# Kernel tuning notes

Hardware: AMD Instinct MI355X
Metric: run time of the kernel (lower is better)

Reference implementation:

```python
import jax, jax.numpy as jnp
import numpy as np
from jax import lax

NUM_FILTERS = 180
DN = ('NCHW', 'OIHW', 'NCHW')


def _gabor_kernel(freq, theta, sigma_x, sigma_y, n_stds=3):
    # real part of skimage.filters.gabor_kernel
    ct, st = np.cos(theta), np.sin(theta)
    x0 = int(np.ceil(max(abs(n_stds * sigma_x * ct), abs(n_stds * sigma_y * st), 1)))
    y0 = int(np.ceil(max(abs(n_stds * sigma_y * ct), abs(n_stds * sigma_x * st), 1)))
    y, x = np.mgrid[-y0:y0 + 1, -x0:x0 + 1]
    rotx = x * ct + y * st
    roty = -x * st + y * ct
    g = np.exp(-0.5 * (rotx ** 2 / sigma_x ** 2 + roty ** 2 / sigma_y ** 2))
    g /= 2.0 * np.pi * sigma_x * sigma_y
    return g * np.cos(2.0 * np.pi * freq * rotx)  # Re{exp(1j*2*pi*f*rotx)}


def _make_weights(sigma_x, sigma_y, freq, num_filters):
    kernels = [
        _gabor_kernel(freq, theta=np.pi - th, sigma_x=sigma_x, sigma_y=sigma_y)
        for th in np.linspace(0, np.pi * (num_filters - 1) / num_filters, num_filters)
    ]
    s = max(max(k.shape) for k in kernels)  # 17 for defaults
    kernels = np.stack([
        np.pad(k, [[(s - k.shape[0]) // 2], [(s - k.shape[1]) // 2]]) for k in kernels
    ])
    return kernels.astype(np.float32)


def _gauss1d(sigma, truncate=4.0):
    # matches scipy.ndimage gaussian kernel (skimage default truncate=4.0)
    r = int(truncate * sigma + 0.5)
    xs = np.arange(-r, r + 1, dtype=np.float64)
    k = np.exp(-0.5 * (xs / sigma) ** 2)
    return (k / k.sum()).astype(np.float32), r


def _gaussian_blur(img, sigma):
    # separable blur with edge-replicate ('nearest') padding, img: [B,1,H,W]
    k, r = _gauss1d(sigma)
    kh = jnp.asarray(k).reshape(1, 1, -1, 1)
    kw = jnp.asarray(k).reshape(1, 1, 1, -1)
    p = jnp.pad(img, ((0, 0), (0, 0), (r, r), (0, 0)), mode='edge')
    img = lax.conv_general_dilated(p, kh, (1, 1), 'VALID', dimension_numbers=DN)
    p = jnp.pad(img, ((0, 0), (0, 0), (0, 0), (r, r)), mode='edge')
    return lax.conv_general_dilated(p, kw, (1, 1), 'VALID', dimension_numbers=DN)


def setup_inputs() -> dict:
    key = jax.random.key(0)
    x = jax.random.uniform(key, (2, 3, 512, 512), dtype=jnp.float32)
    weights = jnp.asarray(_make_weights(1.8, 2.4, 0.23, NUM_FILTERS))[:, None, :, :]  # [180,1,17,17]
    bins = jnp.asarray(
        np.linspace(0, np.pi * (NUM_FILTERS - 1) / NUM_FILTERS, NUM_FILTERS), jnp.float32
    ).reshape(1, -1, 1, 1)
    return {'x': x, 'weights': weights, 'bins': bins}


def reference(x, weights, bins):
    # rgb -> gray, [B,1,H,W]
    gray = (0.2989 * x[:, 0] + 0.587 * x[:, 1] + 0.114 * x[:, 2])[:, None]
    # difference of gaussians (skimage, low=0.4, high=10.0)
    filtered = _gaussian_blur(gray, 0.4) - _gaussian_blur(gray, 10.0)
    kh, kw = weights.shape[2], weights.shape[3]
    response = lax.conv_general_dilated(
        filtered, weights, (1, 1), ((kh // 2, kh // 2), (kw // 2, kw // 2)),
        dimension_numbers=DN)  # [B,180,H,W]
    response = jnp.abs(response)
    idx = jnp.argmax(response, axis=1)[:, None]  # [B,1,H,W]
    orientation_map = idx.astype(jnp.float32) / NUM_FILTERS * 255.0
    orientation_map_rad = orientation_map / NUM_FILTERS * jnp.pi
    d0 = jnp.abs(orientation_map_rad - bins)
    dists = jnp.minimum(d0, jnp.minimum(jnp.abs(orientation_map_rad - bins - jnp.pi),
                                        jnp.abs(orientation_map_rad - bins + jnp.pi)))
    F_orients_norm = response / jnp.sum(response, axis=1, keepdims=True)
    confidence_map = jnp.sum(dists ** 2 * F_orients_norm, axis=1)  # [B,H,W]
    return orientation_map, confidence_map
```

## Files before the change

### kernel.cpp

```cpp
#include <hip/hip_runtime.h>
#include <math.h>
#include <stdint.h>

#define H 512
#define W 512
#define NPIX (H * W)
#define NB 2
#define NF 180
#define KS 17
#define WSCALE 1024.0f

#define RAW_OFF 0
#define BB_OFF  1600
#define BCH_U32 3072
#define PH_U32  (2 * BCH_U32)
#define POOL_U32 (1600 + 2 * PH_U32)

typedef _Float16 half8 __attribute__((ext_vector_type(8)));
typedef float floatx16 __attribute__((ext_vector_type(16)));
typedef uint32_t u32x4 __attribute__((ext_vector_type(4)));

union FragU { u32x4 u; half8 h; };

__device__ inline void gl_lds16(const uint32_t* g, uint32_t* l) {
  __builtin_amdgcn_global_load_lds((const __attribute__((address_space(1))) void*)g,
                                   (__attribute__((address_space(3))) void*)l, 16, 0, 0);
}

__global__ void k_taps(float* __restrict__ taps) {
  if (threadIdx.x == 0 && blockIdx.x == 0) {
    {
      double k[5], s = 0.0;
      for (int i = 0; i < 5; i++) { double xv = (double)(i - 2) / 0.4; k[i] = exp(-0.5 * xv * xv); s += k[i]; }
      for (int i = 0; i < 5; i++) taps[i] = (float)(k[i] / s);
    }
    {
      double k[81], s = 0.0;
      for (int i = 0; i < 81; i++) { double xv = (double)(i - 40) / 10.0; k[i] = exp(-0.5 * xv * xv); s += k[i]; }
      for (int i = 0; i < 81; i++) taps[8 + i] = (float)(k[i] / s);
    }
  }
}

__global__ void k_repackB(const float* __restrict__ w, uint32_t* __restrict__ Bf) {
  int tid = blockIdx.x * 256 + threadIdx.x;
  if (tid >= 19 * 6 * 64 * 4) return;
  int q = tid & 3;
  int lane = (tid >> 2) & 63;
  int ct = tid >> 8;
  int t = ct % 6, c = ct / 6;
  int n = t * 32 + (lane & 31);
  int hf = lane >> 5;
  uint32_t hv = 0, lv = 0;
  for (int s = 0; s < 2; s++) {
    int j = 2 * q + s;
    int k = hf * 8 + j;
    float val = 0.f;
    if (n < NF) {
      if (c < 17)       val = w[n * 289 + c * 17 + k];
      else if (c == 17) val = w[n * 289 + k * 17 + 16];
      else if (k == 0)  val = w[n * 289 + 16 * 17 + 16];
    }
    val *= WSCALE;
    _Float16 hh = (_Float16)val;
    _Float16 ll = (_Float16)(val - (float)hh);
    hv |= (uint32_t)__builtin_bit_cast(uint16_t, hh) << (16 * s);
    lv |= (uint32_t)__builtin_bit_cast(uint16_t, ll) << (16 * s);
  }
  int base = c * 3072;
  int off = t * 256 + lane * 4 + q;
  Bf[base + off] = hv;
  Bf[base + 1536 + off] = lv;
}

__global__ void k_gray(const float* __restrict__ x, float* __restrict__ gray) {
  int i = blockIdx.x * blockDim.x + threadIdx.x;
  if (i >= NB * NPIX) return;
  int b = i / NPIX, r = i % NPIX;
  const float* xb = x + (size_t)b * 3 * NPIX;
  gray[i] = 0.2989f * xb[r] + 0.587f * xb[NPIX + r] + 0.114f * xb[2 * NPIX + r];
}

__global__ void k_vblur2(const float* __restrict__ in, float* __restrict__ outA,
                         float* __restrict__ outB, const float* __restrict__ taps) {
  int i = blockIdx.x * blockDim.x + threadIdx.x;
  if (i >= NB * NPIX) return;
  int b = i / NPIX, r = i % NPIX;
  int y = r / W, xx = r % W;
  const float* img = in + (size_t)b * NPIX;
  float a = 0.f;
#pragma unroll
  for (int j = -2; j <= 2; j++) {
    int yy = y + j; yy = yy < 0 ? 0 : (yy > H - 1 ? H - 1 : yy);
    a = fmaf(taps[j + 2], img[yy * W + xx], a);
  }
  float c = 0.f;
  for (int j = -40; j <= 40; j++) {
    int yy = y + j; yy = yy < 0 ? 0 : (yy > H - 1 ? H - 1 : yy);
    c = fmaf(taps[8 + j + 40], img[yy * W + xx], c);
  }
  outA[i] = a;
  outB[i] = c;
}

__global__ void k_hblur_dog(const float* __restrict__ inA, const float* __restrict__ inB,
                            uint32_t* __restrict__ dogp, const float* __restrict__ taps) {
  int i = blockIdx.x * blockDim.x + threadIdx.x;
  if (i >= NB * NPIX) return;
  int b = i / NPIX, r = i % NPIX;
  int y = r / W, xx = r % W;
  const float* ra = inA + (size_t)b * NPIX + (size_t)y * W;
  const float* rb = inB + (size_t)b * NPIX + (size_t)y * W;
  float a = 0.f;
#pragma unroll
  for (int j = -2; j <= 2; j++) {
    int xc = xx + j; xc = xc < 0 ? 0 : (xc > W - 1 ? W - 1 : xc);
    a = fmaf(taps[j + 2], ra[xc], a);
  }
  float c = 0.f;
  for (int j = -40; j <= 40; j++) {
    int xc = xx + j; xc = xc < 0 ? 0 : (xc > W - 1 ? W - 1 : xc);
    c = fmaf(taps[8 + j + 40], rb[xc], c);
  }
  float d = a - c;
  _Float16 hh = (_Float16)d;
  _Float16 ll = (_Float16)(d - (float)hh);
  dogp[i] = ((uint32_t)__builtin_bit_cast(uint16_t, ll) << 16) |
            (uint32_t)__builtin_bit_cast(uint16_t, hh);
}

__launch_bounds__(256, 1)
__global__ void k_conv(const uint32_t* __restrict__ dogp,
                       const uint32_t* __restrict__ Bf,
                       const float* __restrict__ bins,
                       float* __restrict__ out) {
  __shared__ uint32_t pool[POOL_U32];

  const int b  = blockIdx.z;
  const int y0 = blockIdx.y * 4;
  const int x0 = blockIdx.x * 64;
  const int tid = threadIdx.x;
  const int lane = tid & 63;
  const int w  = __builtin_amdgcn_readfirstlane(tid >> 6);
  const int rp2 = (w >> 1) * 2;
  const int ch  = w & 1;
  const int nl = lane & 31;
  const int half = lane >> 5;

  const uint32_t* dgb = dogp + (size_t)b * NPIX;
  for (int i = tid; i < 20 * 80; i += 256) {
    int ry = i / 80, rx = i % 80;
    int gy = y0 + ry - 8, gx = x0 + rx - 8;
    uint32_t v = 0;
    if (gy >= 0 && gy < H && gx >= 0 && gx < W) v = dgb[gy * W + gx];
    pool[RAW_OFF + i] = v;
  }
  {
    const uint32_t* src = Bf + (size_t)tid * 4;
    uint32_t* dst = &pool[BB_OFF + tid * 4];
#pragma unroll
    for (int i = 0; i < 6; i++) gl_lds16(src + i * 1024, dst + i * 1024);
  }
  asm volatile("s_waitcnt vmcnt(0)" ::: "memory");
  __syncthreads();

  floatx16 acc[2][6];
#pragma unroll
  for (int d = 0; d < 2; d++)
#pragma unroll
    for (int t = 0; t < 6; t++)
#pragma unroll
      for (int q = 0; q < 16; q++) acc[d][t][q] = 0.f;

  const int abase = ch * 32 + nl + half * 8;

  auto buildRow = [&](int tr, FragU& fh, FragU& fl) {
    const uint32_t* rp = &pool[RAW_OFF + tr * 80 + abase];
    uint32_t d[8];
#pragma unroll
    for (int j = 0; j < 8; j++) d[j] = rp[j];
#pragma unroll
    for (int q = 0; q < 4; q++) {
      fh.u[q] = __builtin_amdgcn_perm(d[2 * q + 1], d[2 * q], 0x05040100u);
      fl.u[q] = __builtin_amdgcn_perm(d[2 * q + 1], d[2 * q], 0x07060302u);
    }
  };
  auto buildStrip = [&](int c, int rb, FragU& fh, FragU& fl) {
    int kyb = (c - 17) * 16 + half * 8;
    uint32_t d[8];
#pragma unroll
    for (int j = 0; j < 8; j++) {
      int ky = kyb + j; if (ky > 16) ky = 16;
      d[j] = pool[RAW_OFF + (rb + ky) * 80 + ch * 32 + nl + 16];
    }
#pragma unroll
    for (int q = 0; q < 4; q++) {
      fh.u[q] = __builtin_amdgcn_perm(d[2 * q + 1], d[2 * q], 0x05040100u);
      fl.u[q] = __builtin_amdgcn_perm(d[2 * q + 1], d[2 * q], 0x07060302u);
    }
  };
  auto halfChunk = [&](int off, int t0, FragU& d0h, FragU& d0l, FragU& d1h, FragU& d1l) {
    FragU wh[3], wl[3];
#pragma unroll
    for (int t = 0; t < 3; t++) {
      wh[t].u = *(const u32x4*)&pool[off + (t0 + t) * 256 + lane * 4];
      wl[t].u = *(const u32x4*)&pool[off + 1536 + (t0 + t) * 256 + lane * 4];
    }
#pragma unroll
    for (int t = 0; t < 3; t++) {
      acc[0][t0 + t] = __builtin_amdgcn_mfma_f32_32x32x16_f16(wh[t].h, d0h.h, acc[0][t0 + t], 0, 0, 0);
      acc[1][t0 + t] = __builtin_amdgcn_mfma_f32_32x32x16_f16(wh[t].h, d1h.h, acc[1][t0 + t], 0, 0, 0);
    }
#pragma unroll
    for (int t = 0; t < 3; t++) {
      acc[0][t0 + t] = __builtin_amdgcn_mfma_f32_32x32x16_f16(wh[t].h, d0l.h, acc[0][t0 + t], 0, 0, 0);
      acc[1][t0 + t] = __builtin_amdgcn_mfma_f32_32x32x16_f16(wh[t].h, d1l.h, acc[1][t0 + t], 0, 0, 0);
    }
#pragma unroll
    for (int t = 0; t < 3; t++) {
      acc[0][t0 + t] = __builtin_amdgcn_mfma_f32_32x32x16_f16(wl[t].h, d0h.h, acc[0][t0 + t], 0, 0, 0);
      acc[1][t0 + t] = __builtin_amdgcn_mfma_f32_32x32x16_f16(wl[t].h, d1h.h, acc[1][t0 + t], 0, 0, 0);
    }
  };
  auto mfmaChunk = [&](int off, FragU& d0h, FragU& d0l, FragU& d1h, FragU& d1l) {
    halfChunk(off, 0, d0h, d0l, d1h, d1l);
    halfChunk(off, 3, d0h, d0l, d1h, d1l);
  };

  FragU a0h, a0l, a1h, a1l;
  buildRow(rp2, a0h, a0l);

  int buf = 0;
  for (int p = 0; p < 8; p++) {
    {
      const uint32_t* src = Bf + (size_t)(2 * p + 2) * BCH_U32 + (size_t)tid * 4;
      uint32_t* dst = &pool[BB_OFF + (buf ^ 1) * PH_U32 + tid * 4];
#pragma unroll
      for (int i = 0; i < 6; i++) gl_lds16(src + i * 1024, dst + i * 1024);
    }
    buildRow(rp2 + 1 + 2 * p, a1h, a1l);
    mfmaChunk(BB_OFF + buf * PH_U32, a0h, a0l, a1h, a1l);
    a0h = a1h; a0l = a1l;
    buildRow(rp2 + 2 + 2 * p, a1h, a1l);
    mfmaChunk(BB_OFF + buf * PH_U32 + BCH_U32, a0h, a0l, a1h, a1l);
    a0h = a1h; a0l = a1l;

    asm volatile("s_waitcnt vmcnt(0)" ::: "memory");
    __syncthreads();
    buf ^= 1;
  }

  {
    const uint32_t* src = Bf + (size_t)18 * BCH_U32 + (size_t)tid * 4;
    uint32_t* dst = &pool[BB_OFF + (buf ^ 1) * PH_U32 + tid * 4];
#pragma unroll
    for (int i = 0; i < 3; i++) gl_lds16(src + i * 1024, dst + i * 1024);

    buildRow(rp2 + 17, a1h, a1l);
    mfmaChunk(BB_OFF + buf * PH_U32, a0h, a0l, a1h, a1l);

    FragU s0h, s0l, s1h, s1l;
    buildStrip(17, rp2, s0h, s0l);
    buildStrip(17, rp2 + 1, s1h, s1l);
    mfmaChunk(BB_OFF + buf * PH_U32 + BCH_U32, s0h, s0l, s1h, s1l);

    asm volatile("s_waitcnt vmcnt(0)" ::: "memory");
    __syncthreads();
    buf ^= 1;
  }
  {
    FragU s0h, s0l, s1h, s1l;
    buildStrip(18, rp2, s0h, s0l);
    buildStrip(18, rp2 + 1, s1h, s1l);
    mfmaChunk(BB_OFF + buf * PH_U32, s0h, s0l, s1h, s1l);
  }

  const float PI_F = 3.14159265358979323846f;
  const float INV_PI = 0.31830988618379067154f;
  const double STEPD = 3.14159265358979323846 * 179.0 / 180.0 / 179.0;
  const float stepf = (float)STEPD;
  const float hbase = (4.0f * (float)half) * stepf;

#pragma unroll
  for (int d = 0; d < 2; d++) {
    float m = -1.f; int n = 0; float S0 = 0.f, S1 = 0.f;
#pragma unroll
    for (int t = 0; t < 6; t++) {
#pragma unroll
      for (int q = 0; q < 16; q++) {
        float v = fabsf(acc[d][t][q]);
        if (q & 1) S1 += v; else S0 += v;
        int nf = 32 * t + (q & 3) + 8 * (q >> 2) + 4 * half;
        if (v > m) { m = v; n = nf; }
      }
    }
    float S = S0 + S1;
    {
      float mo = __shfl_xor(m, 32);
      int   no = __shfl_xor(n, 32);
      float So = __shfl_xor(S, 32);
      bool take = (mo > m) || (mo == m && no < n);
      if (take) { m = mo; n = no; }
      S += So;
    }
    float om  = (float)n / 180.0f * 255.0f;
    float rad = om / 180.0f * PI_F;
    float ddc = rad - hbase;
    float C0 = 0.f, C1 = 0.f;
#pragma unroll
    for (int t = 0; t < 6; t++) {
#pragma unroll
      for (int q = 0; q < 16; q++) {
        const float K = (float)((double)(32 * t + (q & 3) + 8 * (q >> 2)) * STEPD);
        float dd = ddc - K;
        float r = rintf(dd * INV_PI);
        float dist = fmaf(-PI_F, r, dd);
        float w2 = dist * dist;
        if (q & 1) C1 = fmaf(w2, fabsf(acc[d][t][q]), C1);
        else       C0 = fmaf(w2, fabsf(acc[d][t][q]), C0);
      }
    }
    float C = C0 + C1;
    C += __shfl_xor(C, 32);
    if (half == 0) {
      int y = y0 + rp2 + d;
      int x = x0 + ch * 32 + nl;
      out[(size_t)b * NPIX + (size_t)y * W + x] = om;
      out[(size_t)NB * NPIX + (size_t)b * NPIX + (size_t)y * W + x] = C / S;
    }
  }
}

extern "C" void kernel_launch(void* const* d_in, const int* in_sizes, int n_in,
                              void* d_out, int out_size, void* d_ws, size_t ws_size,
                              hipStream_t stream) {
  const float* x = (const float*)d_in[0];
  const float* wts = (const float*)d_in[1];
  const float* bins = (const float*)d_in[2];
  float* out = (float*)d_out;

  float* ws = (float*)d_ws;
  float* gray = ws;
  float* tmpA = ws + (size_t)NB * NPIX;
  float* tmpB = tmpA + (size_t)NB * NPIX;
  uint32_t* dogp = (uint32_t*)(tmpB + (size_t)NB * NPIX);
  float* taps = (float*)(dogp + (size_t)NB * NPIX);
  uint32_t* Bf = (uint32_t*)(taps + 128);

  k_taps<<<1, 64, 0, stream>>>(taps);
  k_repackB<<<114, 256, 0, stream>>>(wts, Bf);

  int n = NB * NPIX;
  int blk = 256, grd = (n + blk - 1) / blk;
  k_gray<<<grd, blk, 0, stream>>>(x, gray);
  k_vblur2<<<grd, blk, 0, stream>>>(gray, tmpA, tmpB, taps);
  k_hblur_dog<<<grd, blk, 0, stream>>>(tmpA, tmpB, dogp, taps);

  dim3 g(W / 64, H / 4, NB);
  k_conv<<<g, 256, 0, stream>>>(dogp, Bf, bins, out);
}
```

Baseline: 200.4 us.

## Split filter bank across two wave groups with LDS cross-wave reduction

The conv kernel now runs 512 threads per block, and each wave handles half of the 180 filters (3 of the 6 MFMA tiles) instead of all of them. This halves the accumulator registers per wave and doubles the wave count, which should raise occupancy and latency hiding. The price is an LDS-based argmax/sum merge between filter groups and extra block barriers. The weight staging loads are redistributed across the larger thread count.

Measured after the change: 193.8 us. 3.3% less time.

```diff
diff --git a/kernel.cpp b/kernel.cpp
--- a/kernel.cpp
+++ b/kernel.cpp
@@ -129,7 +129,7 @@
             (uint32_t)__builtin_bit_cast(uint16_t, hh);
 }
 
-__launch_bounds__(256, 1)
+__launch_bounds__(512, 2)
 __global__ void k_conv(const uint32_t* __restrict__ dogp,
                        const uint32_t* __restrict__ Bf,
                        const float* __restrict__ bins,
@@ -142,13 +142,14 @@
   const int tid = threadIdx.x;
   const int lane = tid & 63;
   const int w  = __builtin_amdgcn_readfirstlane(tid >> 6);
-  const int rp2 = (w >> 1) * 2;
-  const int ch  = w & 1;
+  const int fg  = w & 1;
+  const int ch  = (w >> 1) & 1;
+  const int rp2 = (w >> 2) * 2;
   const int nl = lane & 31;
   const int half = lane >> 5;
 
   const uint32_t* dgb = dogp + (size_t)b * NPIX;
-  for (int i = tid; i < 20 * 80; i += 256) {
+  for (int i = tid; i < 20 * 80; i += 512) {
     int ry = i / 80, rx = i % 80;
     int gy = y0 + ry - 8, gx = x0 + rx - 8;
     uint32_t v = 0;
@@ -159,16 +160,16 @@
     const uint32_t* src = Bf + (size_t)tid * 4;
     uint32_t* dst = &pool[BB_OFF + tid * 4];
 #pragma unroll
-    for (int i = 0; i < 6; i++) gl_lds16(src + i * 1024, dst + i * 1024);
+    for (int i = 0; i < 3; i++) gl_lds16(src + i * 2048, dst + i * 2048);
   }
   asm volatile("s_waitcnt vmcnt(0)" ::: "memory");
   __syncthreads();
 
-  floatx16 acc[2][6];
+  floatx16 acc[2][3];
 #pragma unroll
   for (int d = 0; d < 2; d++)
 #pragma unroll
-    for (int t = 0; t < 6; t++)
+    for (int t = 0; t < 3; t++)
 #pragma unroll
       for (int q = 0; q < 16; q++) acc[d][t][q] = 0.f;
 
@@ -199,32 +200,28 @@
       fl.u[q] = __builtin_amdgcn_perm(d[2 * q + 1], d[2 * q], 0x07060302u);
     }
   };
-  auto halfChunk = [&](int off, int t0, FragU& d0h, FragU& d0l, FragU& d1h, FragU& d1l) {
+  auto mfmaChunk = [&](int off, FragU& d0h, FragU& d0l, FragU& d1h, FragU& d1l) {
     FragU wh[3], wl[3];
 #pragma unroll
     for (int t = 0; t < 3; t++) {
-      wh[t].u = *(const u32x4*)&pool[off + (t0 + t) * 256 + lane * 4];
-      wl[t].u = *(const u32x4*)&pool[off + 1536 + (t0 + t) * 256 + lane * 4];
-    }
-#pragma unroll
-    for (int t = 0; t < 3; t++) {
-      acc[0][t0 + t] = __builtin_amdgcn_mfma_f32_32x32x16_f16(wh[t].h, d0h.h, acc[0][t0 + t], 0, 0, 0);
-      acc[1][t0 + t] = __builtin_amdgcn_mfma_f32_32x32x16_f16(wh[t].h, d1h.h, acc[1][t0 + t], 0, 0, 0);
-    }
-#pragma unroll
-    for (int t = 0; t < 3; t++) {
-      acc[0][t0 + t] = __builtin_amdgcn_mfma_f32_32x32x16_f16(wh[t].h, d0l.h, acc[0][t0 + t], 0, 0, 0);
-      acc[1][t0 + t] = __builtin_amdgcn_mfma_f32_32x32x16_f16(wh[t].h, d1l.h, acc[1][t0 + t], 0, 0, 0);
-    }
-#pragma unroll
-    for (int t = 0; t < 3; t++) {
-      acc[0][t0 + t] = __builtin_amdgcn_mfma_f32_32x32x16_f16(wl[t].h, d0h.h, acc[0][t0 + t], 0, 0, 0);
-      acc[1][t0 + t] = __builtin_amdgcn_mfma_f32_32x32x16_f16(wl[t].h, d1h.h, acc[1][t0 + t], 0, 0, 0);
-    }
-  };
-  auto mfmaChunk = [&](int off, FragU& d0h, FragU& d0l, FragU& d1h, FragU& d1l) {
-    halfChunk(off, 0, d0h, d0l, d1h, d1l);
-    halfChunk(off, 3, d0h, d0l, d1h, d1l);
+      wh[t].u = *(const u32x4*)&pool[off + (3 * fg + t) * 256 + lane * 4];
+      wl[t].u = *(const u32x4*)&pool[off + 1536 + (3 * fg + t) * 256 + lane * 4];
+    }
+#pragma unroll
+    for (int t = 0; t < 3; t++) {
+      acc[0][t] = __builtin_amdgcn_mfma_f32_32x32x16_f16(wh[t].h, d0h.h, acc[0][t], 0, 0, 0);
+      acc[1][t] = __builtin_amdgcn_mfma_f32_32x32x16_f16(wh[t].h, d1h.h, acc[1][t], 0, 0, 0);
+    }
+#pragma unroll
+    for (int t = 0; t < 3; t++) {
+      acc[0][t] = __builtin_amdgcn_mfma_f32_32x32x16_f16(wh[t].h, d0l.h, acc[0][t], 0, 0, 0);
+      acc[1][t] = __builtin_amdgcn_mfma_f32_32x32x16_f16(wh[t].h, d1l.h, acc[1][t], 0, 0, 0);
+    }
+#pragma unroll
+    for (int t = 0; t < 3; t++) {
+      acc[0][t] = __builtin_amdgcn_mfma_f32_32x32x16_f16(wl[t].h, d0h.h, acc[0][t], 0, 0, 0);
+      acc[1][t] = __builtin_amdgcn_mfma_f32_32x32x16_f16(wl[t].h, d1h.h, acc[1][t], 0, 0, 0);
+    }
   };
 
   FragU a0h, a0l, a1h, a1l;
@@ -236,7 +233,7 @@
       const uint32_t* src = Bf + (size_t)(2 * p + 2) * BCH_U32 + (size_t)tid * 4;
       uint32_t* dst = &pool[BB_OFF + (buf ^ 1) * PH_U32 + tid * 4];
 #pragma unroll
-      for (int i = 0; i < 6; i++) gl_lds16(src + i * 1024, dst + i * 1024);
+      for (int i = 0; i < 3; i++) gl_lds16(src + i * 2048, dst + i * 2048);
     }
     buildRow(rp2 + 1 + 2 * p, a1h, a1l);
     mfmaChunk(BB_OFF + buf * PH_U32, a0h, a0l, a1h, a1l);
@@ -253,8 +250,8 @@
   {
     const uint32_t* src = Bf + (size_t)18 * BCH_U32 + (size_t)tid * 4;
     uint32_t* dst = &pool[BB_OFF + (buf ^ 1) * PH_U32 + tid * 4];
-#pragma unroll
-    for (int i = 0; i < 3; i++) gl_lds16(src + i * 1024, dst + i * 1024);
+    gl_lds16(src, dst);
+    if (tid < 256) gl_lds16(src + 2048, dst + 2048);
 
     buildRow(rp2 + 17, a1h, a1l);
     mfmaChunk(BB_OFF + buf * PH_U32, a0h, a0l, a1h, a1l);
@@ -274,44 +271,80 @@
     buildStrip(18, rp2 + 1, s1h, s1l);
     mfmaChunk(BB_OFF + buf * PH_U32, s0h, s0l, s1h, s1l);
   }
+  __syncthreads();
+
+  float* pm = (float*)&pool[0];
+  int*   pn = (int*)&pool[512];
+  float* pS = (float*)&pool[1024];
+  float* pc = (float*)&pool[1536];
+  int*   fn = (int*)&pool[2048];
+  float* fS = (float*)&pool[2304];
 
   const float PI_F = 3.14159265358979323846f;
   const float INV_PI = 0.31830988618379067154f;
   const double STEPD = 3.14159265358979323846 * 179.0 / 180.0 / 179.0;
   const float stepf = (float)STEPD;
   const float hbase = (4.0f * (float)half) * stepf;
+  const int colp = ch * 32 + nl;
 
 #pragma unroll
   for (int d = 0; d < 2; d++) {
     float m = -1.f; int n = 0; float S0 = 0.f, S1 = 0.f;
 #pragma unroll
-    for (int t = 0; t < 6; t++) {
+    for (int t = 0; t < 3; t++) {
 #pragma unroll
       for (int q = 0; q < 16; q++) {
         float v = fabsf(acc[d][t][q]);
         if (q & 1) S1 += v; else S0 += v;
-        int nf = 32 * t + (q & 3) + 8 * (q >> 2) + 4 * half;
+        int nf = 32 * (3 * fg + t) + (q & 3) + 8 * (q >> 2) + 4 * half;
         if (v > m) { m = v; n = nf; }
       }
     }
     float S = S0 + S1;
-    {
-      float mo = __shfl_xor(m, 32);
-      int   no = __shfl_xor(n, 32);
-      float So = __shfl_xor(S, 32);
-      bool take = (mo > m) || (mo == m && no < n);
-      if (take) { m = mo; n = no; }
-      S += So;
-    }
-    float om  = (float)n / 180.0f * 255.0f;
+    float mo = __shfl_xor(m, 32);
+    int   no = __shfl_xor(n, 32);
+    float So = __shfl_xor(S, 32);
+    bool take = (mo > m) || (mo == m && no < n);
+    if (take) { m = mo; n = no; }
+    S += So;
+    if (half == 0) {
+      int o = ((rp2 + d) * 2 + fg) * 64 + colp;
+      pm[o] = m; pn[o] = n; pS[o] = S;
+    }
+  }
+  __syncthreads();
+
+  if (fg == 0) {
+#pragma unroll
+    for (int d = 0; d < 2; d++) {
+      int rd = rp2 + d;
+      int o0 = (rd * 2 + 0) * 64 + colp;
+      int o1 = (rd * 2 + 1) * 64 + colp;
+      float m0 = pm[o0], m1 = pm[o1];
+      int n = (m1 > m0) ? pn[o1] : pn[o0];
+      float S = pS[o0] + pS[o1];
+      float om = (float)n / 180.0f * 255.0f;
+      if (half == 0) {
+        fn[rd * 64 + colp] = n; fS[rd * 64 + colp] = S;
+        out[(size_t)b * NPIX + (size_t)(y0 + rd) * W + x0 + colp] = om;
+      }
+    }
+  }
+  __syncthreads();
+
+#pragma unroll
+  for (int d = 0; d < 2; d++) {
+    int rd = rp2 + d;
+    int nwin = fn[rd * 64 + colp];
+    float om = (float)nwin / 180.0f * 255.0f;
     float rad = om / 180.0f * PI_F;
     float ddc = rad - hbase;
     float C0 = 0.f, C1 = 0.f;
 #pragma unroll
-    for (int t = 0; t < 6; t++) {
+    for (int t = 0; t < 3; t++) {
 #pragma unroll
       for (int q = 0; q < 16; q++) {
-        const float K = (float)((double)(32 * t + (q & 3) + 8 * (q >> 2)) * STEPD);
+        const float K = (float)((double)(32 * (3 * fg + t) + (q & 3) + 8 * (q >> 2)) * STEPD);
         float dd = ddc - K;
         float r = rintf(dd * INV_PI);
         float dist = fmaf(-PI_F, r, dd);
@@ -322,11 +355,19 @@
     }
     float C = C0 + C1;
     C += __shfl_xor(C, 32);
-    if (half == 0) {
-      int y = y0 + rp2 + d;
-      int x = x0 + ch * 32 + nl;
-      out[(size_t)b * NPIX + (size_t)y * W + x] = om;
-      out[(size_t)NB * NPIX + (size_t)b * NPIX + (size_t)y * W + x] = C / S;
+    if (half == 0) pc[(rd * 2 + fg) * 64 + colp] = C;
+  }
+  __syncthreads();
+
+  if (fg == 0) {
+#pragma unroll
+    for (int d = 0; d < 2; d++) {
+      int rd = rp2 + d;
+      float C = pc[(rd * 2 + 0) * 64 + colp] + pc[(rd * 2 + 1) * 64 + colp];
+      if (half == 0) {
+        out[(size_t)NB * NPIX + (size_t)b * NPIX + (size_t)(y0 + rd) * W + x0 + colp]
+            = C / fS[rd * 64 + colp];
+      }
     }
   }
 }
@@ -357,5 +398,5 @@
   k_hblur_dog<<<grd, blk, 0, stream>>>(tmpA, tmpB, dogp, taps);
 
   dim3 g(W / 64, H / 4, NB);
-  k_conv<<<g, 256, 0, stream>>>(dogp, Bf, bins, out);
-}
+  k_conv<<<g, 512, 0, stream>>>(dogp, Bf, bins, out);
+}
```
